# Performance work log

Measured on AMD Instinct MI355X. Metric: run time of the kernel, lower is better.

The kernel has to match this reference:

```python
import jax, jax.numpy as jnp
import numpy as np

B, T, H, DK = 4, 2048, 16, 64
F = H * DK
CK, NL = 64, 16  # chunk_size, num left chunks
MIN_VAL = float(np.finfo(np.float16).min)


def chunk_mask(size, ck, nl):
    # row i attends cols [max((i//ck - nl)*ck, 0), (i//ck + 1)*ck)
    i = jnp.arange(size)
    start = jnp.maximum((i // ck - nl) * ck, 0)
    end = (i // ck + 1) * ck
    j = jnp.arange(size)
    return (j[None, :] >= start[:, None]) & (j[None, :] < end[:, None])


def setup_inputs() -> dict:
    rng = jax.random.key(0)
    ks = jax.random.split(rng, 14)
    s = 1.0 / np.sqrt(F)
    mask = jnp.broadcast_to(chunk_mask(T, CK, NL)[None], (B, T, T))  # padding mask all-True & chunk band
    return {
        "query": jax.random.normal(ks[0], (B, T, F), jnp.float32),
        "key": jax.random.normal(ks[1], (B, T, F), jnp.float32),
        "value": jax.random.normal(ks[2], (B, T, F), jnp.float32),
        "pos_emb": jax.random.normal(ks[3], (1, T, F), jnp.float32),
        "mask": mask,
        "Wq": jax.random.normal(ks[4], (F, F), jnp.float32) * s,
        "bq": jnp.zeros((F,), jnp.float32),
        "Wk": jax.random.normal(ks[5], (F, F), jnp.float32) * s,
        "bk": jnp.zeros((F,), jnp.float32),
        "Wv": jax.random.normal(ks[6], (F, F), jnp.float32) * s,
        "bv": jnp.zeros((F,), jnp.float32),
        "Wp": jax.random.normal(ks[7], (F, F), jnp.float32) * s,
        "Wo": jax.random.normal(ks[8], (F, F), jnp.float32) * s,
        "bo": jnp.zeros((F,), jnp.float32),
        "pos_bias_u": jax.random.normal(ks[9], (H, DK), jnp.float32) * 0.05,
        "pos_bias_v": jax.random.normal(ks[10], (H, DK), jnp.float32) * 0.05,
    }


def reference(query, key, value, pos_emb, mask, Wq, bq, Wk, bk, Wv, bv, Wp, Wo, bo, pos_bias_u, pos_bias_v):
    b, t1, _ = query.shape
    t2 = key.shape[1]
    q = (query @ Wq.T + bq).reshape(b, t1, H, DK)            # (b, t1, h, d)
    k = (key @ Wk.T + bk).reshape(b, t2, H, DK).transpose(0, 2, 1, 3)   # (b, h, t2, d)
    v = (value @ Wv.T + bv).reshape(b, t2, H, DK).transpose(0, 2, 1, 3)  # (b, h, t2, d)
    p = (pos_emb @ Wp.T).reshape(pos_emb.shape[0], -1, H, DK).transpose(0, 2, 1, 3)[0]  # (h, t2, d)
    # matrix_ac: content score with bias u; matrix_bd: position score with bias v (no rel_shift in forward)
    matrix_ac = jnp.einsum('bthd,bhsd->bhts', q + pos_bias_u, k)
    matrix_bd = jnp.einsum('bthd,hsd->bhts', q + pos_bias_v, p)
    scores = (matrix_ac + matrix_bd) / np.sqrt(DK)
    m = mask[:, None, :, :]                                   # (b, 1, t1, t2)
    scores = jnp.where(m, scores, MIN_VAL)
    attn = jax.nn.softmax(scores, axis=-1)
    attn = jnp.where(m, attn, 0.0)
    x = jnp.einsum('bhts,bhsd->bthd', attn, v).reshape(b, t1, F)
    return x @ Wo.T + bo
```

## Files before the change

### kernel.cpp

```cpp
#include <hip/hip_runtime.h>
#include <hip/hip_bf16.h>

#define B_ 4
#define T_ 2048
#define H_ 16
#define DK_ 64
#define F_ 1024
#define SCALE_LOG2 0.18033688011112042f

typedef __bf16 bf16x8 __attribute__((ext_vector_type(8)));
typedef __bf16 bf16x4 __attribute__((ext_vector_type(4)));
typedef float f32x4 __attribute__((ext_vector_type(4)));

__device__ __forceinline__ void async_cp16(const void* g, void* l) {
  __builtin_amdgcn_global_load_lds((const __attribute__((address_space(1))) void*)g,
                                   (__attribute__((address_space(3))) void*)l, 16, 0, 0);
}

struct CvtArgs {
  const float* src[9];
  __bf16* dst[9];
  int n[9];
};
__global__ void cvt_all(CvtArgs a) {
  int t = blockIdx.y;
  int i = (blockIdx.x * 256 + threadIdx.x) * 8;
  if (i >= a.n[t]) return;
  const float* in = a.src[t];
  __bf16* out = a.dst[t];
  float4 x = *(const float4*)(in + i);
  float4 y = *(const float4*)(in + i + 4);
  bf16x8 o;
  o[0] = (__bf16)x.x; o[1] = (__bf16)x.y; o[2] = (__bf16)x.z; o[3] = (__bf16)x.w;
  o[4] = (__bf16)y.x; o[5] = (__bf16)y.y; o[6] = (__bf16)y.z; o[7] = (__bf16)y.w;
  *(bf16x8*)(out + i) = o;
}

struct GemmQKVP {
  const __bf16* W[4];
  const __bf16* Act[4];
  const float* bias[4];
  __bf16* out[4];
  int Nblocks[4];
};
__global__ __launch_bounds__(256) void gemm_qkvp(GemmQKVP g) {
  const int z = blockIdx.z;
  if ((int)blockIdx.x >= g.Nblocks[z]) return;
  const __bf16* __restrict__ A = g.W[z];
  const __bf16* __restrict__ Bm = g.Act[z];
  const float* __restrict__ bias = g.bias[z];
  __bf16* __restrict__ Cout = g.out[z];
  constexpr int K = F_;
  __shared__ __bf16 As[128 * 32];
  __shared__ __bf16 Bs[128 * 32];
  const int tid = threadIdx.x;
  const int wave = tid >> 6, lane = tid & 63;
  const int mrow = lane & 15, quad = lane >> 4;
  const long m0 = (long)blockIdx.y * 128;
  const long n0 = (long)blockIdx.x * 128;
  const int wr = (wave >> 1) * 64, wc = (wave & 1) * 64;
  const int srow = lane >> 2;
  const int scol = (lane & 3) * 8;
  f32x4 acc[4][4] = {};
  for (int k0 = 0; k0 < K; k0 += 32) {
    if (k0) __syncthreads();
    for (int ph = 0; ph < 2; ++ph) {
      int rb = ph * 64 + wave * 16;
      async_cp16(A + (m0 + rb + srow) * (long)K + k0 + scol, As + rb * 32);
      async_cp16(Bm + (n0 + rb + srow) * (long)K + k0 + scol, Bs + rb * 32);
    }
    __syncthreads();
    bf16x8 af[4], bf[4];
    for (int i = 0; i < 4; i++) af[i] = *(const bf16x8*)&As[(wr + i * 16 + mrow) * 32 + quad * 8];
    for (int j = 0; j < 4; j++) bf[j] = *(const bf16x8*)&Bs[(wc + j * 16 + mrow) * 32 + quad * 8];
    for (int i = 0; i < 4; i++)
      for (int j = 0; j < 4; j++)
        acc[i][j] = __builtin_amdgcn_mfma_f32_16x16x32_bf16(af[i], bf[j], acc[i][j], 0, 0, 0);
  }
  for (int i = 0; i < 4; i++) {
    int frow = (int)m0 + wr + i * 16 + quad * 4;
    float4 b4 = bias ? *(const float4*)&bias[frow] : make_float4(0.f, 0.f, 0.f, 0.f);
    int h = frow >> 6, dbase = frow & 63;
    for (int j = 0; j < 4; j++) {
      int token = (int)n0 + wc + j * 16 + mrow;
      int bb = token >> 11, tt = token & 2047;
      bf16x4 pk;
      pk[0] = (__bf16)(acc[i][j][0] + b4.x);
      pk[1] = (__bf16)(acc[i][j][1] + b4.y);
      pk[2] = (__bf16)(acc[i][j][2] + b4.z);
      pk[3] = (__bf16)(acc[i][j][3] + b4.w);
      *(bf16x4*)&Cout[(((long)(bb * H_ + h)) * T_ + tt) * DK_ + dbase] = pk;
    }
  }
}

__global__ __launch_bounds__(256) void gemm_out(
    const __bf16* __restrict__ A, const __bf16* __restrict__ Bm,
    float* __restrict__ Cout, const float* __restrict__ bias, int N, int K) {
  __shared__ __bf16 As[128 * 32];
  __shared__ __bf16 Bs[128 * 32];
  const int tid = threadIdx.x;
  const int wave = tid >> 6, lane = tid & 63;
  const int mrow = lane & 15, quad = lane >> 4;
  const long m0 = (long)blockIdx.y * 128, n0 = (long)blockIdx.x * 128;
  const int wr = (wave >> 1) * 64, wc = (wave & 1) * 64;
  const int srow = lane >> 2;
  const int scol = (lane & 3) * 8;
  f32x4 acc[4][4] = {};
  for (int k0 = 0; k0 < K; k0 += 32) {
    if (k0) __syncthreads();
    for (int ph = 0; ph < 2; ++ph) {
      int rb = ph * 64 + wave * 16;
      async_cp16(A + (m0 + rb + srow) * (long)K + k0 + scol, As + rb * 32);
      async_cp16(Bm + (n0 + rb + srow) * (long)K + k0 + scol, Bs + rb * 32);
    }
    __syncthreads();
    bf16x8 af[4], bf[4];
    for (int i = 0; i < 4; i++) af[i] = *(const bf16x8*)&As[(wr + i * 16 + mrow) * 32 + quad * 8];
    for (int j = 0; j < 4; j++) bf[j] = *(const bf16x8*)&Bs[(wc + j * 16 + mrow) * 32 + quad * 8];
    for (int i = 0; i < 4; i++)
      for (int j = 0; j < 4; j++)
        acc[i][j] = __builtin_amdgcn_mfma_f32_16x16x32_bf16(af[i], bf[j], acc[i][j], 0, 0, 0);
  }
  for (int i = 0; i < 4; i++) {
    int row = (int)m0 + wr + i * 16 + quad * 4;
    for (int j = 0; j < 4; j++) {
      int col = (int)n0 + wc + j * 16 + mrow;
      float bval = bias[col];
      for (int r = 0; r < 4; r++)
        Cout[(long)(row + r) * N + col] = acc[i][j][r] + bval;
    }
  }
}

__global__ __launch_bounds__(256) void prep(
    const __bf16* __restrict__ Ph, __bf16* __restrict__ Kh,
    const __bf16* __restrict__ Vh, __bf16* __restrict__ Vth,
    const float* __restrict__ u, const float* __restrict__ vb,
    float* __restrict__ biasC) {
  __shared__ __bf16 Vl[64 * 72];
  const int tc = blockIdx.x, h = blockIdx.y, b = blockIdx.z;
  const int tid = threadIdx.x;
  const int r4 = tid >> 2, c16 = (tid & 3) * 16;
  const long bh = b * H_ + h;
  const long kbase = (bh * T_ + tc * 64 + r4) * DK_ + c16;
  const long pbase = (((long)h) * T_ + tc * 64 + r4) * DK_ + c16;
  bf16x8 k0 = *(const bf16x8*)&Kh[kbase];
  bf16x8 k1 = *(const bf16x8*)&Kh[kbase + 8];
  bf16x8 p0 = *(const bf16x8*)&Ph[pbase];
  bf16x8 p1 = *(const bf16x8*)&Ph[pbase + 8];
  float4 u0 = *(const float4*)&u[h * 64 + c16];
  float4 u1 = *(const float4*)&u[h * 64 + c16 + 4];
  float4 u2 = *(const float4*)&u[h * 64 + c16 + 8];
  float4 u3 = *(const float4*)&u[h * 64 + c16 + 12];
  float4 v0 = *(const float4*)&vb[h * 64 + c16];
  float4 v1 = *(const float4*)&vb[h * 64 + c16 + 4];
  float4 v2 = *(const float4*)&vb[h * 64 + c16 + 8];
  float4 v3 = *(const float4*)&vb[h * 64 + c16 + 12];
  float s = 0.f;
  {
    const float uu[16] = {u0.x,u0.y,u0.z,u0.w,u1.x,u1.y,u1.z,u1.w,u2.x,u2.y,u2.z,u2.w,u3.x,u3.y,u3.z,u3.w};
    const float vv[16] = {v0.x,v0.y,v0.z,v0.w,v1.x,v1.y,v1.z,v1.w,v2.x,v2.y,v2.z,v2.w,v3.x,v3.y,v3.z,v3.w};
#pragma unroll
    for (int j = 0; j < 8; j++) {
      s += (float)k0[j] * uu[j] + (float)p0[j] * vv[j];
      s += (float)k1[j] * uu[8 + j] + (float)p1[j] * vv[8 + j];
    }
  }
  bf16x8 kp0, kp1;
#pragma unroll
  for (int j = 0; j < 8; j++) {
    kp0[j] = (__bf16)((float)k0[j] + (float)p0[j]);
    kp1[j] = (__bf16)((float)k1[j] + (float)p1[j]);
  }
  *(bf16x8*)&Kh[kbase] = kp0;
  *(bf16x8*)&Kh[kbase + 8] = kp1;
  s += __shfl_xor(s, 1);
  s += __shfl_xor(s, 2);
  if ((tid & 3) == 0) biasC[bh * T_ + tc * 64 + r4] = s * SCALE_LOG2;
  const long vbase = (bh * T_ + tc * 64 + r4) * DK_ + c16;
  bf16x8 vv0 = *(const bf16x8*)&Vh[vbase];
  bf16x8 vv1 = *(const bf16x8*)&Vh[vbase + 8];
  *(bf16x8*)&Vl[r4 * 72 + c16] = vv0;
  *(bf16x8*)&Vl[r4 * 72 + c16 + 8] = vv1;
  __syncthreads();
  const int d4 = tid >> 2, tcol = (tid & 3) * 16;
  bf16x8 o0, o1;
#pragma unroll
  for (int j = 0; j < 8; j++) {
    o0[j] = Vl[(tcol + j) * 72 + d4];
    o1[j] = Vl[(tcol + 8 + j) * 72 + d4];
  }
  long obase = (bh * DK_ + d4) * T_ + tc * 64 + tcol;
  *(bf16x8*)&Vth[obase] = o0;
  *(bf16x8*)&Vth[obase + 8] = o1;
}

template <int FULL>
__device__ __forceinline__ void attn_step2(
    int s0, long bh, int tid, int wave, int mrow, int quad,
    const __bf16* __restrict__ Kh, const __bf16* __restrict__ Vth,
    const float* __restrict__ Bp, const bf16x8 (&qf)[4][2],
    __bf16* Pl, __bf16* Vt, f32x4 accO[4], f32x4& accL) {
  __syncthreads();
  if (FULL) {
#pragma unroll
    for (int p = 0; p < 4; ++p) {
      int idx = tid + p * 256;
      int row = idx >> 4, colg = (idx & 15) * 8;
      *(bf16x8*)&Vt[row * 136 + colg] =
          *(const bf16x8*)&Vth[(bh * DK_ + row) * T_ + s0 + colg];
    }
  } else {
#pragma unroll
    for (int p = 0; p < 2; ++p) {
      int idx = tid + p * 256;
      int row = idx >> 3, colg = (idx & 7) * 8;
      *(bf16x8*)&Vt[row * 136 + colg] =
          *(const bf16x8*)&Vth[(bh * DK_ + row) * T_ + s0 + colg];
    }
  }
  if (FULL || wave < 2) {
    const int krow = s0 + wave * 32;
    bf16x8 kf[2][2];
#pragma unroll
    for (int nt = 0; nt < 2; ++nt)
#pragma unroll
      for (int kh = 0; kh < 2; ++kh)
        kf[nt][kh] = *(const bf16x8*)&Kh[(bh * T_ + krow + nt * 16 + mrow) * DK_ + kh * 32 + quad * 8];
    float bias01[2] = {Bp[krow + mrow], Bp[krow + 16 + mrow]};
    f32x4 s[4][2];
#pragma unroll
    for (int mt = 0; mt < 4; ++mt)
#pragma unroll
      for (int nt = 0; nt < 2; ++nt) {
        f32x4 a = {0.f, 0.f, 0.f, 0.f};
        a = __builtin_amdgcn_mfma_f32_16x16x32_bf16(qf[mt][0], kf[nt][0], a, 0, 0, 0);
        a = __builtin_amdgcn_mfma_f32_16x16x32_bf16(qf[mt][1], kf[nt][1], a, 0, 0, 0);
        s[mt][nt] = a;
      }
#pragma unroll
    for (int mt = 0; mt < 4; ++mt)
#pragma unroll
      for (int nt = 0; nt < 2; ++nt)
#pragma unroll
        for (int r = 0; r < 4; ++r) {
          float p = __builtin_amdgcn_exp2f(s[mt][nt][r] * SCALE_LOG2 + bias01[nt]);
          Pl[(mt * 16 + quad * 4 + r) * 136 + wave * 32 + nt * 16 + mrow] = (__bf16)p;
        }
  }
  __syncthreads();
  constexpr int NKT = FULL ? 4 : 2;
  bf16x8 ones;
#pragma unroll
  for (int j = 0; j < 8; ++j) ones[j] = (__bf16)1.0f;
  bf16x8 ap[NKT];
#pragma unroll
  for (int kt = 0; kt < NKT; ++kt)
    ap[kt] = *(const bf16x8*)&Pl[(wave * 16 + mrow) * 136 + kt * 32 + quad * 8];
#pragma unroll
  for (int kt = 0; kt < NKT; ++kt) {
    accL = __builtin_amdgcn_mfma_f32_16x16x32_bf16(ap[kt], ones, accL, 0, 0, 0);
#pragma unroll
    for (int nt = 0; nt < 4; ++nt) {
      bf16x8 bv = *(const bf16x8*)&Vt[(nt * 16 + mrow) * 136 + kt * 32 + quad * 8];
      accO[nt] = __builtin_amdgcn_mfma_f32_16x16x32_bf16(ap[kt], bv, accO[nt], 0, 0, 0);
    }
  }
}

__global__ __launch_bounds__(256) void attn_banded(
    const __bf16* __restrict__ Qh, const __bf16* __restrict__ Kh,
    const __bf16* __restrict__ Vth, const float* __restrict__ biasC,
    __bf16* __restrict__ X) {
  __shared__ __bf16 Pl[64 * 136];
  __shared__ __bf16 Vt[64 * 136];
  const int qc = blockIdx.x, h = blockIdx.y, b = blockIdx.z;
  const int tid = threadIdx.x, wave = tid >> 6, lane = tid & 63;
  const int mrow = lane & 15, quad = lane >> 4;
  const long bh = b * H_ + h;
  const int span = (qc >= 16 ? 17 : qc + 1);
  const int s_lo = (qc + 1 - span) * 64, s_hi = (qc + 1) * 64;
  const float* Bp = biasC + bh * T_;
  bf16x8 qf[4][2];
#pragma unroll
  for (int mt = 0; mt < 4; ++mt)
#pragma unroll
    for (int kh = 0; kh < 2; ++kh)
      qf[mt][kh] = *(const bf16x8*)&Qh[(bh * T_ + qc * 64 + mt * 16 + mrow) * DK_ + kh * 32 + quad * 8];
  f32x4 accO[4] = {};
  f32x4 accL = {0.f, 0.f, 0.f, 0.f};
  int s0 = s_lo;
  if (span & 1) {
    attn_step2<0>(s0, bh, tid, wave, mrow, quad, Kh, Vth, Bp, qf, Pl, Vt, accO, accL);
    s0 += 64;
  }
  for (; s0 < s_hi; s0 += 128)
    attn_step2<1>(s0, bh, tid, wave, mrow, quad, Kh, Vth, Bp, qf, Pl, Vt, accO, accL);
#pragma unroll
  for (int r = 0; r < 4; ++r) {
    float inv = 1.0f / accL[r];
    int t = qc * 64 + wave * 16 + quad * 4 + r;
#pragma unroll
    for (int nt = 0; nt < 4; ++nt)
      X[((long)(b * T_ + t) * H_ + h) * DK_ + nt * 16 + mrow] = (__bf16)(accO[nt][r] * inv);
  }
}

extern "C" void kernel_launch(void* const* d_in, const int* in_sizes, int n_in,
                              void* d_out, int out_size, void* d_ws, size_t ws_size,
                              hipStream_t stream) {
  (void)in_sizes; (void)n_in; (void)out_size; (void)ws_size;
  const float* query = (const float*)d_in[0];
  const float* key   = (const float*)d_in[1];
  const float* value = (const float*)d_in[2];
  const float* pos   = (const float*)d_in[3];
  const float* Wq = (const float*)d_in[5];
  const float* bq = (const float*)d_in[6];
  const float* Wk = (const float*)d_in[7];
  const float* bk = (const float*)d_in[8];
  const float* Wv = (const float*)d_in[9];
  const float* bv = (const float*)d_in[10];
  const float* Wp = (const float*)d_in[11];
  const float* Wo = (const float*)d_in[12];
  const float* bo = (const float*)d_in[13];
  const float* pu = (const float*)d_in[14];
  const float* pvb = (const float*)d_in[15];

  const long NQ = (long)B_ * T_ * F_;
  const long NP = (long)T_ * F_;
  const long NW = (long)F_ * F_;
  char* ws = (char*)d_ws;
  __bf16* qb  = (__bf16*)ws; ws += NQ * 2;
  __bf16* kb  = (__bf16*)ws; ws += NQ * 2;
  __bf16* vbm = (__bf16*)ws; ws += NQ * 2;
  __bf16* pb  = (__bf16*)ws; ws += NP * 2;
  __bf16* wqb = (__bf16*)ws; ws += NW * 2;
  __bf16* wkb = (__bf16*)ws; ws += NW * 2;
  __bf16* wvb = (__bf16*)ws; ws += NW * 2;
  __bf16* wpb = (__bf16*)ws; ws += NW * 2;
  __bf16* wob = (__bf16*)ws; ws += NW * 2;
  __bf16* Qh  = (__bf16*)ws; ws += NQ * 2;
  __bf16* Kh  = (__bf16*)ws; ws += NQ * 2;
  __bf16* Vh  = (__bf16*)ws; ws += NQ * 2;
  __bf16* Ph  = (__bf16*)ws; ws += NP * 2;
  float*  biasC = (float*)ws; ws += (long)B_ * H_ * T_ * 4;
  __bf16* Vth = kb;
  __bf16* Xb  = qb;

  {
    CvtArgs ca;
    ca.src[0] = query; ca.dst[0] = qb;  ca.n[0] = (int)NQ;
    ca.src[1] = key;   ca.dst[1] = kb;  ca.n[1] = (int)NQ;
    ca.src[2] = value; ca.dst[2] = vbm; ca.n[2] = (int)NQ;
    ca.src[3] = pos;   ca.dst[3] = pb;  ca.n[3] = (int)NP;
    ca.src[4] = Wq;    ca.dst[4] = wqb; ca.n[4] = (int)NW;
    ca.src[5] = Wk;    ca.dst[5] = wkb; ca.n[5] = (int)NW;
    ca.src[6] = Wv;    ca.dst[6] = wvb; ca.n[6] = (int)NW;
    ca.src[7] = Wp;    ca.dst[7] = wpb; ca.n[7] = (int)NW;
    ca.src[8] = Wo;    ca.dst[8] = wob; ca.n[8] = (int)NW;
    cvt_all<<<dim3(4096, 9), 256, 0, stream>>>(ca);
  }
  {
    GemmQKVP g;
    g.W[0] = wqb; g.Act[0] = qb;  g.bias[0] = bq;      g.out[0] = Qh; g.Nblocks[0] = 64;
    g.W[1] = wkb; g.Act[1] = kb;  g.bias[1] = bk;      g.out[1] = Kh; g.Nblocks[1] = 64;
    g.W[2] = wvb; g.Act[2] = vbm; g.bias[2] = bv;      g.out[2] = Vh; g.Nblocks[2] = 64;
    g.W[3] = wpb; g.Act[3] = pb;  g.bias[3] = nullptr; g.out[3] = Ph; g.Nblocks[3] = 16;
    gemm_qkvp<<<dim3(64, 8, 4), 256, 0, stream>>>(g);
  }
  prep<<<dim3(32, 16, 4), 256, 0, stream>>>(Ph, Kh, Vh, Vth, pu, pvb, biasC);
  attn_banded<<<dim3(32, 16, 4), 256, 0, stream>>>(Qh, Kh, Vth, biasC, Xb);
  gemm_out<<<dim3(8, 64), 256, 0, stream>>>(Xb, wob, (float*)d_out, bo, F_, F_);
}
```

Baseline: 422.9 us.

## Fuse K/P add, bias dot products and V transpose into projection GEMM epilogues

```diff
diff --git a/kernel.cpp b/kernel.cpp
--- a/kernel.cpp
+++ b/kernel.cpp
@@ -36,21 +36,26 @@
   *(bf16x8*)(out + i) = o;
 }
 
-struct GemmQKVP {
-  const __bf16* W[4];
-  const __bf16* Act[4];
-  const float* bias[4];
-  __bf16* out[4];
-  int Nblocks[4];
-};
-__global__ __launch_bounds__(256) void gemm_qkvp(GemmQKVP g) {
-  const int z = blockIdx.z;
-  if ((int)blockIdx.x >= g.Nblocks[z]) return;
-  const __bf16* __restrict__ A = g.W[z];
-  const __bf16* __restrict__ Bm = g.Act[z];
-  const float* __restrict__ bias = g.bias[z];
-  __bf16* __restrict__ Cout = g.out[z];
-  constexpr int K = F_;
+#define GEMM_MAIN_LOOP(A_, B_ptr, AsP, BsP)                                              \
+  for (int k0 = 0; k0 < F_; k0 += 32) {                                                  \
+    if (k0) __syncthreads();                                                             \
+    for (int ph = 0; ph < 2; ++ph) {                                                     \
+      int rb = ph * 64 + wave * 16;                                                      \
+      async_cp16(A_ + (m0 + rb + srow) * (long)F_ + k0 + scol, AsP + rb * 32);           \
+      async_cp16(B_ptr + (n0 + rb + srow) * (long)F_ + k0 + scol, BsP + rb * 32);        \
+    }                                                                                    \
+    __syncthreads();                                                                     \
+    bf16x8 af[4], bfr[4];                                                                \
+    for (int i = 0; i < 4; i++) af[i] = *(const bf16x8*)&AsP[(wr + i * 16 + mrow) * 32 + quad * 8]; \
+    for (int j = 0; j < 4; j++) bfr[j] = *(const bf16x8*)&BsP[(wc + j * 16 + mrow) * 32 + quad * 8]; \
+    for (int i = 0; i < 4; i++)                                                          \
+      for (int j = 0; j < 4; j++)                                                        \
+        acc[i][j] = __builtin_amdgcn_mfma_f32_16x16x32_bf16(af[i], bfr[j], acc[i][j], 0, 0, 0); \
+  }
+
+__global__ __launch_bounds__(256) void gemm_p(
+    const __bf16* __restrict__ Wm, const __bf16* __restrict__ Act,
+    __bf16* __restrict__ Ph, const float* __restrict__ vb, float* __restrict__ pbias) {
   __shared__ __bf16 As[128 * 32];
   __shared__ __bf16 Bs[128 * 32];
   const int tid = threadIdx.x;
@@ -59,44 +64,147 @@
   const long m0 = (long)blockIdx.y * 128;
   const long n0 = (long)blockIdx.x * 128;
   const int wr = (wave >> 1) * 64, wc = (wave & 1) * 64;
-  const int srow = lane >> 2;
-  const int scol = (lane & 3) * 8;
+  const int srow = lane >> 2, scol = (lane & 3) * 8;
   f32x4 acc[4][4] = {};
-  for (int k0 = 0; k0 < K; k0 += 32) {
-    if (k0) __syncthreads();
-    for (int ph = 0; ph < 2; ++ph) {
-      int rb = ph * 64 + wave * 16;
-      async_cp16(A + (m0 + rb + srow) * (long)K + k0 + scol, As + rb * 32);
-      async_cp16(Bm + (n0 + rb + srow) * (long)K + k0 + scol, Bs + rb * 32);
-    }
-    __syncthreads();
-    bf16x8 af[4], bf[4];
-    for (int i = 0; i < 4; i++) af[i] = *(const bf16x8*)&As[(wr + i * 16 + mrow) * 32 + quad * 8];
-    for (int j = 0; j < 4; j++) bf[j] = *(const bf16x8*)&Bs[(wc + j * 16 + mrow) * 32 + quad * 8];
-    for (int i = 0; i < 4; i++)
-      for (int j = 0; j < 4; j++)
-        acc[i][j] = __builtin_amdgcn_mfma_f32_16x16x32_bf16(af[i], bf[j], acc[i][j], 0, 0, 0);
-  }
+  GEMM_MAIN_LOOP(Wm, Act, As, Bs)
+  const int h = ((int)m0 + wr) >> 6;
+  float s[4] = {0.f, 0.f, 0.f, 0.f};
   for (int i = 0; i < 4; i++) {
     int frow = (int)m0 + wr + i * 16 + quad * 4;
-    float4 b4 = bias ? *(const float4*)&bias[frow] : make_float4(0.f, 0.f, 0.f, 0.f);
-    int h = frow >> 6, dbase = frow & 63;
+    float4 v4 = *(const float4*)&vb[frow];
+    int dbase = frow & 63;
     for (int j = 0; j < 4; j++) {
       int token = (int)n0 + wc + j * 16 + mrow;
-      int bb = token >> 11, tt = token & 2047;
+      s[j] += v4.x * acc[i][j][0] + v4.y * acc[i][j][1] + v4.z * acc[i][j][2] + v4.w * acc[i][j][3];
       bf16x4 pk;
-      pk[0] = (__bf16)(acc[i][j][0] + b4.x);
-      pk[1] = (__bf16)(acc[i][j][1] + b4.y);
-      pk[2] = (__bf16)(acc[i][j][2] + b4.z);
-      pk[3] = (__bf16)(acc[i][j][3] + b4.w);
-      *(bf16x4*)&Cout[(((long)(bb * H_ + h)) * T_ + tt) * DK_ + dbase] = pk;
+      pk[0] = (__bf16)acc[i][j][0]; pk[1] = (__bf16)acc[i][j][1];
+      pk[2] = (__bf16)acc[i][j][2]; pk[3] = (__bf16)acc[i][j][3];
+      *(bf16x4*)&Ph[((long)h * T_ + token) * DK_ + dbase] = pk;
+    }
+  }
+  for (int j = 0; j < 4; j++) {
+    float t = s[j];
+    t += __shfl_xor(t, 16);
+    t += __shfl_xor(t, 32);
+    if (quad == 0) {
+      int token = (int)n0 + wc + j * 16 + mrow;
+      pbias[h * T_ + token] = t;
+    }
+  }
+}
+
+struct GemmQKV {
+  const __bf16* W[3];
+  const __bf16* Act[3];
+  const float* bias[3];
+};
+__global__ __launch_bounds__(256) void gemm_qkv(
+    GemmQKV g, const __bf16* __restrict__ Ph, const float* __restrict__ u,
+    const float* __restrict__ pbias, __bf16* __restrict__ Qh, __bf16* __restrict__ Kh,
+    __bf16* __restrict__ Vth, float* __restrict__ biasC) {
+  __shared__ __align__(16) __bf16 smem[128 * 132];
+  __bf16* As = smem;
+  __bf16* Bs = smem + 128 * 32;
+  const int z = blockIdx.z;
+  const __bf16* __restrict__ A = g.W[z];
+  const __bf16* __restrict__ Bact = g.Act[z];
+  const float* __restrict__ bias = g.bias[z];
+  const int tid = threadIdx.x;
+  const int wave = tid >> 6, lane = tid & 63;
+  const int mrow = lane & 15, quad = lane >> 4;
+  const long m0 = (long)blockIdx.y * 128;
+  const long n0 = (long)blockIdx.x * 128;
+  const int wr = (wave >> 1) * 64, wc = (wave & 1) * 64;
+  const int srow = lane >> 2, scol = (lane & 3) * 8;
+  f32x4 acc[4][4] = {};
+  GEMM_MAIN_LOOP(A, Bact, As, Bs)
+  const int h = ((int)m0 + wr) >> 6;
+  const int bb = (int)(n0 >> 11);
+
+  if (z == 0) {
+    for (int i = 0; i < 4; i++) {
+      int frow = (int)m0 + wr + i * 16 + quad * 4;
+      float4 b4 = *(const float4*)&bias[frow];
+      int dbase = frow & 63;
+      for (int j = 0; j < 4; j++) {
+        int token = (int)n0 + wc + j * 16 + mrow;
+        int tt = token & 2047;
+        bf16x4 pk;
+        pk[0] = (__bf16)(acc[i][j][0] + b4.x);
+        pk[1] = (__bf16)(acc[i][j][1] + b4.y);
+        pk[2] = (__bf16)(acc[i][j][2] + b4.z);
+        pk[3] = (__bf16)(acc[i][j][3] + b4.w);
+        *(bf16x4*)&Qh[(((long)(bb * H_ + h)) * T_ + tt) * DK_ + dbase] = pk;
+      }
+    }
+  } else if (z == 1) {
+    float s[4] = {0.f, 0.f, 0.f, 0.f};
+    for (int i = 0; i < 4; i++) {
+      int frow = (int)m0 + wr + i * 16 + quad * 4;
+      float4 b4 = *(const float4*)&bias[frow];
+      float4 u4 = *(const float4*)&u[frow];
+      int dbase = frow & 63;
+      for (int j = 0; j < 4; j++) {
+        int token = (int)n0 + wc + j * 16 + mrow;
+        int tt = token & 2047;
+        float k0v = acc[i][j][0] + b4.x;
+        float k1v = acc[i][j][1] + b4.y;
+        float k2v = acc[i][j][2] + b4.z;
+        float k3v = acc[i][j][3] + b4.w;
+        s[j] += u4.x * k0v + u4.y * k1v + u4.z * k2v + u4.w * k3v;
+        bf16x4 p4 = *(const bf16x4*)&Ph[((long)h * T_ + tt) * DK_ + dbase];
+        bf16x4 pk;
+        pk[0] = (__bf16)(k0v + (float)p4[0]);
+        pk[1] = (__bf16)(k1v + (float)p4[1]);
+        pk[2] = (__bf16)(k2v + (float)p4[2]);
+        pk[3] = (__bf16)(k3v + (float)p4[3]);
+        *(bf16x4*)&Kh[(((long)(bb * H_ + h)) * T_ + tt) * DK_ + dbase] = pk;
+      }
+    }
+    for (int j = 0; j < 4; j++) {
+      float t = s[j];
+      t += __shfl_xor(t, 16);
+      t += __shfl_xor(t, 32);
+      if (quad == 0) {
+        int token = (int)n0 + wc + j * 16 + mrow;
+        int tt = token & 2047;
+        biasC[((long)(bb * H_ + h)) * T_ + tt] = (t + pbias[h * T_ + tt]) * SCALE_LOG2;
+      }
+    }
+  } else {
+    __syncthreads();
+    for (int i = 0; i < 4; i++) {
+      int fl = wr + i * 16 + quad * 4;
+      float4 b4 = *(const float4*)&bias[m0 + fl];
+      for (int j = 0; j < 4; j++) {
+        int tl = wc + j * 16 + mrow;
+        bf16x4 pk;
+        pk[0] = (__bf16)(acc[i][j][0] + b4.x);
+        pk[1] = (__bf16)(acc[i][j][1] + b4.y);
+        pk[2] = (__bf16)(acc[i][j][2] + b4.z);
+        pk[3] = (__bf16)(acc[i][j][3] + b4.w);
+        *(bf16x4*)&smem[tl * 132 + fl] = pk;
+      }
+    }
+    __syncthreads();
+    int t0 = (int)(n0 & 2047);
+#pragma unroll
+    for (int p = 0; p < 8; ++p) {
+      int idx = p * 256 + tid;
+      int dl = idx >> 4, tch = (idx & 15) * 8;
+      bf16x8 o;
+#pragma unroll
+      for (int k = 0; k < 8; ++k) o[k] = smem[(tch + k) * 132 + dl];
+      int hh = ((int)m0 >> 6) + (dl >> 6);
+      int d = dl & 63;
+      *(bf16x8*)&Vth[(((long)(bb * H_ + hh)) * DK_ + d) * T_ + t0 + tch] = o;
     }
   }
 }
 
 __global__ __launch_bounds__(256) void gemm_out(
     const __bf16* __restrict__ A, const __bf16* __restrict__ Bm,
-    float* __restrict__ Cout, const float* __restrict__ bias, int N, int K) {
+    float* __restrict__ Cout, const float* __restrict__ bias, int N) {
   __shared__ __bf16 As[128 * 32];
   __shared__ __bf16 Bs[128 * 32];
   const int tid = threadIdx.x;
@@ -104,24 +212,9 @@
   const int mrow = lane & 15, quad = lane >> 4;
   const long m0 = (long)blockIdx.y * 128, n0 = (long)blockIdx.x * 128;
   const int wr = (wave >> 1) * 64, wc = (wave & 1) * 64;
-  const int srow = lane >> 2;
-  const int scol = (lane & 3) * 8;
+  const int srow = lane >> 2, scol = (lane & 3) * 8;
   f32x4 acc[4][4] = {};
-  for (int k0 = 0; k0 < K; k0 += 32) {
-    if (k0) __syncthreads();
-    for (int ph = 0; ph < 2; ++ph) {
-      int rb = ph * 64 + wave * 16;
-      async_cp16(A + (m0 + rb + srow) * (long)K + k0 + scol, As + rb * 32);
-      async_cp16(Bm + (n0 + rb + srow) * (long)K + k0 + scol, Bs + rb * 32);
-    }
-    __syncthreads();
-    bf16x8 af[4], bf[4];
-    for (int i = 0; i < 4; i++) af[i] = *(const bf16x8*)&As[(wr + i * 16 + mrow) * 32 + quad * 8];
-    for (int j = 0; j < 4; j++) bf[j] = *(const bf16x8*)&Bs[(wc + j * 16 + mrow) * 32 + quad * 8];
-    for (int i = 0; i < 4; i++)
-      for (int j = 0; j < 4; j++)
-        acc[i][j] = __builtin_amdgcn_mfma_f32_16x16x32_bf16(af[i], bf[j], acc[i][j], 0, 0, 0);
-  }
+  GEMM_MAIN_LOOP(A, Bm, As, Bs)
   for (int i = 0; i < 4; i++) {
     int row = (int)m0 + wr + i * 16 + quad * 4;
     for (int j = 0; j < 4; j++) {
@@ -131,69 +224,6 @@
         Cout[(long)(row + r) * N + col] = acc[i][j][r] + bval;
     }
   }
-}
-
-__global__ __launch_bounds__(256) void prep(
-    const __bf16* __restrict__ Ph, __bf16* __restrict__ Kh,
-    const __bf16* __restrict__ Vh, __bf16* __restrict__ Vth,
-    const float* __restrict__ u, const float* __restrict__ vb,
-    float* __restrict__ biasC) {
-  __shared__ __bf16 Vl[64 * 72];
-  const int tc = blockIdx.x, h = blockIdx.y, b = blockIdx.z;
-  const int tid = threadIdx.x;
-  const int r4 = tid >> 2, c16 = (tid & 3) * 16;
-  const long bh = b * H_ + h;
-  const long kbase = (bh * T_ + tc * 64 + r4) * DK_ + c16;
-  const long pbase = (((long)h) * T_ + tc * 64 + r4) * DK_ + c16;
-  bf16x8 k0 = *(const bf16x8*)&Kh[kbase];
-  bf16x8 k1 = *(const bf16x8*)&Kh[kbase + 8];
-  bf16x8 p0 = *(const bf16x8*)&Ph[pbase];
-  bf16x8 p1 = *(const bf16x8*)&Ph[pbase + 8];
-  float4 u0 = *(const float4*)&u[h * 64 + c16];
-  float4 u1 = *(const float4*)&u[h * 64 + c16 + 4];
-  float4 u2 = *(const float4*)&u[h * 64 + c16 + 8];
-  float4 u3 = *(const float4*)&u[h * 64 + c16 + 12];
-  float4 v0 = *(const float4*)&vb[h * 64 + c16];
-  float4 v1 = *(const float4*)&vb[h * 64 + c16 + 4];
-  float4 v2 = *(const float4*)&vb[h * 64 + c16 + 8];
-  float4 v3 = *(const float4*)&vb[h * 64 + c16 + 12];
-  float s = 0.f;
-  {
-    const float uu[16] = {u0.x,u0.y,u0.z,u0.w,u1.x,u1.y,u1.z,u1.w,u2.x,u2.y,u2.z,u2.w,u3.x,u3.y,u3.z,u3.w};
-    const float vv[16] = {v0.x,v0.y,v0.z,v0.w,v1.x,v1.y,v1.z,v1.w,v2.x,v2.y,v2.z,v2.w,v3.x,v3.y,v3.z,v3.w};
-#pragma unroll
-    for (int j = 0; j < 8; j++) {
-      s += (float)k0[j] * uu[j] + (float)p0[j] * vv[j];
-      s += (float)k1[j] * uu[8 + j] + (float)p1[j] * vv[8 + j];
-    }
-  }
-  bf16x8 kp0, kp1;
-#pragma unroll
-  for (int j = 0; j < 8; j++) {
-    kp0[j] = (__bf16)((float)k0[j] + (float)p0[j]);
-    kp1[j] = (__bf16)((float)k1[j] + (float)p1[j]);
-  }
-  *(bf16x8*)&Kh[kbase] = kp0;
-  *(bf16x8*)&Kh[kbase + 8] = kp1;
-  s += __shfl_xor(s, 1);
-  s += __shfl_xor(s, 2);
-  if ((tid & 3) == 0) biasC[bh * T_ + tc * 64 + r4] = s * SCALE_LOG2;
-  const long vbase = (bh * T_ + tc * 64 + r4) * DK_ + c16;
-  bf16x8 vv0 = *(const bf16x8*)&Vh[vbase];
-  bf16x8 vv1 = *(const bf16x8*)&Vh[vbase + 8];
-  *(bf16x8*)&Vl[r4 * 72 + c16] = vv0;
-  *(bf16x8*)&Vl[r4 * 72 + c16 + 8] = vv1;
-  __syncthreads();
-  const int d4 = tid >> 2, tcol = (tid & 3) * 16;
-  bf16x8 o0, o1;
-#pragma unroll
-  for (int j = 0; j < 8; j++) {
-    o0[j] = Vl[(tcol + j) * 72 + d4];
-    o1[j] = Vl[(tcol + 8 + j) * 72 + d4];
-  }
-  long obase = (bh * DK_ + d4) * T_ + tc * 64 + tcol;
-  *(bf16x8*)&Vth[obase] = o0;
-  *(bf16x8*)&Vth[obase + 8] = o1;
 }
 
 template <int FULL>
@@ -342,10 +372,10 @@
   __bf16* wob = (__bf16*)ws; ws += NW * 2;
   __bf16* Qh  = (__bf16*)ws; ws += NQ * 2;
   __bf16* Kh  = (__bf16*)ws; ws += NQ * 2;
-  __bf16* Vh  = (__bf16*)ws; ws += NQ * 2;
+  __bf16* Vth = (__bf16*)ws; ws += NQ * 2;
   __bf16* Ph  = (__bf16*)ws; ws += NP * 2;
   float*  biasC = (float*)ws; ws += (long)B_ * H_ * T_ * 4;
-  __bf16* Vth = kb;
+  float*  pbias = (float*)ws; ws += (long)H_ * T_ * 4;
   __bf16* Xb  = qb;
 
   {
@@ -361,15 +391,14 @@
     ca.src[8] = Wo;    ca.dst[8] = wob; ca.n[8] = (int)NW;
     cvt_all<<<dim3(4096, 9), 256, 0, stream>>>(ca);
   }
+  gemm_p<<<dim3(16, 8), 256, 0, stream>>>(wpb, pb, Ph, pvb, pbias);
   {
-    GemmQKVP g;
-    g.W[0] = wqb; g.Act[0] = qb;  g.bias[0] = bq;      g.out[0] = Qh; g.Nblocks[0] = 64;
-    g.W[1] = wkb; g.Act[1] = kb;  g.bias[1] = bk;      g.out[1] = Kh; g.Nblocks[1] = 64;
-    g.W[2] = wvb; g.Act[2] = vbm; g.bias[2] = bv;      g.out[2] = Vh; g.Nblocks[2] = 64;
-    g.W[3] = wpb; g.Act[3] = pb;  g.bias[3] = nullptr; g.out[3] = Ph; g.Nblocks[3] = 16;
-    gemm_qkvp<<<dim3(64, 8, 4), 256, 0, stream>>>(g);
-  }
-  prep<<<dim3(32, 16, 4), 256, 0, stream>>>(Ph, Kh, Vh, Vth, pu, pvb, biasC);
+    GemmQKV g;
+    g.W[0] = wqb; g.Act[0] = qb;  g.bias[0] = bq;
+    g.W[1] = wkb; g.Act[1] = kb;  g.bias[1] = bk;
+    g.W[2] = wvb; g.Act[2] = vbm; g.bias[2] = bv;
+    gemm_qkv<<<dim3(64, 8, 3), 256, 0, stream>>>(g, Ph, pu, pbias, Qh, Kh, Vth, biasC);
+  }
   attn_banded<<<dim3(32, 16, 4), 256, 0, stream>>>(Qh, Kh, Vth, biasC, Xb);
-  gemm_out<<<dim3(8, 64), 256, 0, stream>>>(Xb, wob, (float*)d_out, bo, F_, F_);
-}
+  gemm_out<<<dim3(8, 64), 256, 0, stream>>>(Xb, wob, (float*)d_out, bo, F_);
+}
```

Result: no change. 423.9 us (+0.2%).
